# Performance work log

Hardware: AMD Instinct MI355X
Metric: run time of the kernel (lower is better)

## Reference

```python
import jax, jax.numpy as jnp
import numpy as np

DEPTH, HEADS, K, EPS = 4, 8, 3, 1e-5
DIM, CIN, COUT = 128, 64, 64


def conv1x1(x, w, b=None):
    y = jnp.einsum('oi,bihw->bohw', w, x)
    return y if b is None else y + b[None, :, None, None]


def dilated_conv3x3(x, w, b, d):
    y = jax.lax.conv_general_dilated(
        x, w, window_strides=(1, 1), padding=[(d, d), (d, d)],
        rhs_dilation=(d, d), dimension_numbers=('NCHW', 'OIHW', 'NCHW'))
    return y + b[None, :, None, None]


def batchnorm_train(x, g, b):
    # BatchNorm2d in training mode: biased batch stats over (B,H,W)
    mu = jnp.mean(x, axis=(0, 2, 3), keepdims=True)
    var = jnp.var(x, axis=(0, 2, 3), keepdims=True)
    return (x - mu) * jax.lax.rsqrt(var + EPS) * g[None, :, None, None] + b[None, :, None, None]


def unfold3(x):
    # nn.Unfold(k=3, pad=1): (B,C,H,W) -> (B,C,k*k,H,W), patch index row-major (dy,dx)
    B, C, H, W = x.shape
    p = K // 2
    xp = jnp.pad(x, ((0, 0), (0, 0), (p, p), (p, p)))
    return jnp.stack([xp[:, :, dy:dy + H, dx:dx + W]
                      for dy in range(K) for dx in range(K)], axis=2)


def local_self_attention(x, qkv_w, fc_w, fc_b):
    B, C, H, W = x.shape
    c = C // HEADS
    scale = c ** -0.5
    qkv = conv1x1(x, qkv_w)                      # (B,3C,H,W)
    q, k, v = jnp.split(qkv, 3, axis=1)
    shape6 = lambda t: unfold3(t).reshape(B, HEADS, c, K * K, H, W)
    q, k, v = shape6(q) * scale, shape6(k), shape6(v)
    # NOTE: original einsum labels dim2 (channels/head) as n/m and dim3 (k^2) as the
    # contracted axis, i.e. channel-attention contracted over the 9 patch positions.
    dots = jnp.einsum('bhnkij,bhmkij->bhnmij', q, k)   # (B,h,c,c,H,W)
    attn = jax.nn.softmax(dots, axis=3)
    out = jnp.einsum('bhnmij,bhmkij->bhnkij', attn, v)  # (B,h,c,k^2,H,W)
    out = out.reshape(B, C, K * K, H, W).sum(axis=2)
    return conv1x1(out, fc_w, fc_b) + x


def setup_inputs() -> dict:
    key = jax.random.key(0)
    ks = jax.random.split(key, 12)
    s = 0.05
    return {
        'x': jax.random.normal(ks[0], (2, CIN, 96, 96), jnp.float32),
        'w_in': jax.random.normal(ks[1], (DIM, CIN), jnp.float32) * s,
        'b_in': jnp.zeros((DIM,), jnp.float32),
        'conv_w': jax.random.normal(ks[2], (DEPTH, DIM, DIM, 3, 3), jnp.float32) * s,
        'conv_b': jnp.zeros((DEPTH, DIM), jnp.float32),
        'bn_g': jnp.ones((DEPTH, DIM), jnp.float32),
        'bn_b': jnp.zeros((DEPTH, DIM), jnp.float32),
        'qkv_w': jax.random.normal(ks[3], (DEPTH, 3 * DIM, DIM), jnp.float32) * s,
        'fc_w': jax.random.normal(ks[4], (DEPTH, DIM, DIM), jnp.float32) * s,
        'fc_b': jnp.zeros((DEPTH, DIM), jnp.float32),
        'w_out': jax.random.normal(ks[5], (COUT, DIM), jnp.float32) * s,
        'b_out': jnp.zeros((COUT,), jnp.float32),
    }


def reference(x, w_in, b_in, conv_w, conv_b, bn_g, bn_b, qkv_w, fc_w, fc_b, w_out, b_out):
    h = conv1x1(x, w_in, b_in)
    for i in range(DEPTH):
        d = 2 ** i
        h = jax.nn.relu(batchnorm_train(dilated_conv3x3(h, conv_w[i], conv_b[i], d), bn_g[i], bn_b[i]))
        h = local_self_attention(h, qkv_w[i], fc_w[i], fc_b[i])
    return conv1x1(h, w_out, b_out)
```

## Files before the change

### kernel.cpp

```cpp
#include <hip/hip_runtime.h>
#include <math.h>

typedef __attribute__((ext_vector_type(8))) short bf16x8;
typedef __attribute__((ext_vector_type(4))) float f32x4;
typedef __attribute__((ext_vector_type(4))) unsigned short us4;
typedef __attribute__((ext_vector_type(8))) unsigned short us8;

constexpr int BB = 2;
constexpr int CC = 128;
constexpr int HH = 96, WW = 96;
constexpr int PP = HH * WW;
constexpr int NN = BB * PP;
constexpr int CONV_BLKS = NN / 48;

__device__ __forceinline__ float bf2f(unsigned short u) {
    return __uint_as_float(((unsigned)u) << 16);
}
__device__ __forceinline__ unsigned short f2bf(float f) {
    unsigned u = __float_as_uint(f);
    unsigned r = u + 0x7fff + ((u >> 16) & 1);
    return (unsigned short)(r >> 16);
}

__global__ __launch_bounds__(256)
void k_wconv(const float* __restrict__ conv_w, const float* __restrict__ qkv_w,
             const float* __restrict__ fc_w, const float* __restrict__ w_in,
             const float* __restrict__ w_out,
             unsigned short* __restrict__ wcv, unsigned short* __restrict__ wqkv,
             unsigned short* __restrict__ wfc, unsigned short* __restrict__ wi,
             unsigned short* __restrict__ wo)
{
    int gid = blockIdx.x * 256 + threadIdx.x;
    if (gid < 589824) {
        int L = gid / 147456, r = gid % 147456;
        int o = r / 1152, k = r % 1152;
        int t = k / 128, c = k % 128;
        float v = conv_w[(((size_t)(L * 128 + o) * 128 + c) * 9) + t];
        wcv[gid] = f2bf(v);
    } else if (gid < 786432) {
        int g = gid - 589824;
        int o = (g % 49152) / 128;
        float v = qkv_w[g] * (o < 128 ? 0.25f : 1.0f);
        wqkv[g] = f2bf(v);
    } else if (gid < 851968) {
        int g = gid - 786432;
        wfc[g] = f2bf(fc_w[g]);
    } else if (gid < 860160) {
        int g = gid - 851968;
        wi[g] = f2bf(w_in[g]);
    } else if (gid < 868352) {
        int g = gid - 860160;
        wo[g] = f2bf(w_out[g]);
    }
}

__global__ __launch_bounds__(256)
void k_xconv(const float* __restrict__ x, unsigned short* __restrict__ xT)
{
    int n = blockIdx.x * 256 + threadIdx.x;
    int b = n / PP, p = n - b * PP;
    unsigned short* dst = xT + (size_t)n * 64;
    #pragma unroll
    for (int cg = 0; cg < 16; ++cg) {
        us4 st;
        #pragma unroll
        for (int r = 0; r < 4; ++r)
            st[r] = f2bf(x[((size_t)(b * 64 + cg * 4 + r)) * PP + p]);
        *reinterpret_cast<us4*>(dst + cg * 4) = st;
    }
}

template<int DIL>
__global__ __launch_bounds__(192)
void k_conv(const unsigned short* __restrict__ W,
            const unsigned short* __restrict__ act,
            float* __restrict__ y,
            float* __restrict__ parts,
            const unsigned short* __restrict__ zp)
{
    int tid = threadIdx.x;
    int lane = tid & 63, wz = tid >> 6;
    int l15 = lane & 15, kg = lane >> 4;

    int n_base = blockIdx.x * 48;
    int o_base = blockIdx.y * 64;

    const unsigned short* wbase[4];
    #pragma unroll
    for (int fm = 0; fm < 4; ++fm)
        wbase[fm] = W + (size_t)(o_base + fm * 16 + l15) * 1152 + kg * 8;

    const unsigned short* bbase[3];
    int iF[3], jF[3];
    #pragma unroll
    for (int fn = 0; fn < 3; ++fn) {
        int n = n_base + fn * 16 + l15;
        bbase[fn] = act + (size_t)n * 128 + kg * 8;
        int pix = n % PP;
        iF[fn] = pix / WW;
        jF[fn] = pix % WW;
    }

    f32x4 acc[4][3];
    #pragma unroll
    for (int fm = 0; fm < 4; ++fm)
        #pragma unroll
        for (int fn = 0; fn < 3; ++fn)
            acc[fm][fn] = (f32x4){0.f, 0.f, 0.f, 0.f};

    const unsigned short* zpk = zp + kg * 8;
    int t0 = wz * 3;
    #pragma unroll
    for (int tt = 0; tt < 3; ++tt) {
        int t = t0 + tt;
        int oy = (t / 3 - 1) * DIL, ox = (t % 3 - 1) * DIL;
        int disp = (oy * WW + ox) * 128;
        const unsigned short* baddr[3];
        #pragma unroll
        for (int fn = 0; fn < 3; ++fn) {
            bool v = ((unsigned)(iF[fn] + oy) < (unsigned)HH) &&
                     ((unsigned)(jF[fn] + ox) < (unsigned)WW);
            baddr[fn] = v ? (bbase[fn] + disp) : zpk;
        }
        #pragma unroll
        for (int c0 = 0; c0 < 128; c0 += 32) {
            bf16x8 a[4], b[3];
            #pragma unroll
            for (int fm = 0; fm < 4; ++fm)
                a[fm] = *reinterpret_cast<const bf16x8*>(wbase[fm] + t * 128 + c0);
            #pragma unroll
            for (int fn = 0; fn < 3; ++fn)
                b[fn] = *reinterpret_cast<const bf16x8*>(baddr[fn] + c0);
            #pragma unroll
            for (int fm = 0; fm < 4; ++fm)
                #pragma unroll
                for (int fn = 0; fn < 3; ++fn)
                    acc[fm][fn] = __builtin_amdgcn_mfma_f32_16x16x32_bf16(
                        a[fm], b[fn], acc[fm][fn], 0, 0, 0);
        }
    }

    __shared__ float red[2][48][64];
    if (wz) {
        #pragma unroll
        for (int fm = 0; fm < 4; ++fm)
            #pragma unroll
            for (int fn = 0; fn < 3; ++fn)
                #pragma unroll
                for (int r = 0; r < 4; ++r)
                    red[wz - 1][fm * 12 + fn * 4 + r][lane] = acc[fm][fn][r];
    }
    __syncthreads();
    if (wz == 0) {
        #pragma unroll
        for (int fm = 0; fm < 4; ++fm)
            #pragma unroll
            for (int fn = 0; fn < 3; ++fn)
                #pragma unroll
                for (int r = 0; r < 4; ++r)
                    acc[fm][fn][r] += red[0][fm * 12 + fn * 4 + r][lane] +
                                      red[1][fm * 12 + fn * 4 + r][lane];

        #pragma unroll
        for (int fm = 0; fm < 4; ++fm) {
            int o0 = o_base + fm * 16 + kg * 4;
            #pragma unroll
            for (int fn = 0; fn < 3; ++fn) {
                int n = n_base + fn * 16 + l15;
                *reinterpret_cast<f32x4*>(y + (size_t)n * 128 + o0) = acc[fm][fn];
            }
        }

        #pragma unroll
        for (int fm = 0; fm < 4; ++fm) {
            #pragma unroll
            for (int r = 0; r < 4; ++r) {
                float s = 0.f, s2 = 0.f;
                #pragma unroll
                for (int fn = 0; fn < 3; ++fn) {
                    float v = acc[fm][fn][r];
                    s += v; s2 += v * v;
                }
                #pragma unroll
                for (int m = 1; m <= 8; m <<= 1) {
                    s  += __shfl_xor(s,  m, 64);
                    s2 += __shfl_xor(s2, m, 64);
                }
                if (l15 == 0) {
                    int c = o_base + fm * 16 + kg * 4 + r;
                    parts[(size_t)blockIdx.x * 256 + c]       = s;
                    parts[(size_t)blockIdx.x * 256 + 128 + c] = s2;
                }
            }
        }
    }
}

template<int WM, int WN, int F, int MODE>
__global__ __launch_bounds__(WM * WN * 64)
void k_gemm(const unsigned short* __restrict__ W,
            const unsigned short* __restrict__ act,
            const float* __restrict__ bias,
            const unsigned short* __restrict__ resid,
            void* __restrict__ outp,
            int Kw, int Cin, int Cout)
{
    int tid = threadIdx.x;
    int lane = tid & 63, wv = tid >> 6;
    int wm = wv % WM, wn = wv / WM;
    int l15 = lane & 15, kg = lane >> 4;

    int n_base = blockIdx.x * (WN * 16 * F) + wn * 16 * F;
    int o_base = blockIdx.y * (WM * 64) + wm * 64;

    const unsigned short* wbase[4];
    #pragma unroll
    for (int fm = 0; fm < 4; ++fm) {
        int o = o_base + fm * 16 + l15;
        wbase[fm] = W + (size_t)o * Kw + kg * 8;
    }

    const unsigned short* bbase[F];
    #pragma unroll
    for (int fn = 0; fn < F; ++fn) {
        int n = n_base + fn * 16 + l15;
        bbase[fn] = act + (size_t)n * Cin + kg * 8;
    }

    f32x4 acc[4][F];
    #pragma unroll
    for (int fm = 0; fm < 4; ++fm)
        #pragma unroll
        for (int fn = 0; fn < F; ++fn)
            acc[fm][fn] = (f32x4){0.f, 0.f, 0.f, 0.f};

    #pragma unroll
    for (int k0 = 0; k0 < 128; k0 += 32) {
        if (k0 >= Cin) break;
        bf16x8 a[4], b[F];
        #pragma unroll
        for (int fm = 0; fm < 4; ++fm)
            a[fm] = *reinterpret_cast<const bf16x8*>(wbase[fm] + k0);
        #pragma unroll
        for (int fn = 0; fn < F; ++fn)
            b[fn] = *reinterpret_cast<const bf16x8*>(bbase[fn] + k0);
        #pragma unroll
        for (int fm = 0; fm < 4; ++fm)
            #pragma unroll
            for (int fn = 0; fn < F; ++fn)
                acc[fm][fn] = __builtin_amdgcn_mfma_f32_16x16x32_bf16(
                    a[fm], b[fn], acc[fm][fn], 0, 0, 0);
    }

    #pragma unroll
    for (int fm = 0; fm < 4; ++fm) {
        #pragma unroll
        for (int fn = 0; fn < F; ++fn) {
            f32x4 v = acc[fm][fn];
            int n = n_base + fn * 16 + l15;
            int o0 = o_base + fm * 16 + kg * 4;
            if constexpr (MODE == 0 || MODE == 2) {
                if (bias) {
                    #pragma unroll
                    for (int r = 0; r < 4; ++r) v[r] += bias[o0 + r];
                }
                if constexpr (MODE == 2) {
                    us4 rv = *reinterpret_cast<const us4*>(resid + (size_t)n * Cout + o0);
                    #pragma unroll
                    for (int r = 0; r < 4; ++r) v[r] += bf2f(rv[r]);
                }
                us4 st;
                #pragma unroll
                for (int r = 0; r < 4; ++r) st[r] = f2bf(v[r]);
                *reinterpret_cast<us4*>((unsigned short*)outp + (size_t)n * Cout + o0) = st;
            } else {
                int b_ = n / PP, p = n - b_ * PP;
                float* op = (float*)outp;
                #pragma unroll
                for (int r = 0; r < 4; ++r)
                    op[((size_t)(b_ * Cout + o0 + r)) * PP + p] = v[r] + bias[o0 + r];
            }
        }
    }
}

__global__ __launch_bounds__(384)
void k_bnfin(const float* __restrict__ partials, const float* __restrict__ g,
             const float* __restrict__ b, float* __restrict__ scsh)
{
    int c = blockIdx.x;
    int t = threadIdx.x;
    float s  = partials[(size_t)t * 256 + c];
    float s2 = partials[(size_t)t * 256 + 128 + c];
    #pragma unroll
    for (int m = 32; m > 0; m >>= 1) {
        s  += __shfl_down(s,  m, 64);
        s2 += __shfl_down(s2, m, 64);
    }
    __shared__ float ls[6], ls2[6];
    int wid = t >> 6;
    if ((t & 63) == 0) { ls[wid] = s; ls2[wid] = s2; }
    __syncthreads();
    if (t == 0) {
        float S = 0.f, S2 = 0.f;
        #pragma unroll
        for (int w = 0; w < 6; ++w) { S += ls[w]; S2 += ls2[w]; }
        const float inv = 1.f / (float)NN;
        float mu = S * inv;
        float var = S2 * inv - mu * mu;
        float sc = g[c] * rsqrtf(var + 1e-5f);
        scsh[c] = sc;
        scsh[128 + c] = b[c] - mu * sc;
    }
}

__global__ __launch_bounds__(256)
void k_bnrelu(const float* __restrict__ y, const float* __restrict__ scsh,
              unsigned short* __restrict__ h)
{
    int gid = blockIdx.x * 256 + threadIdx.x;
    int c0 = (gid * 4) & 127;
    size_t idx = (size_t)gid * 4;
    f32x4 v = *reinterpret_cast<const f32x4*>(y + idx);
    us4 st;
    #pragma unroll
    for (int r = 0; r < 4; ++r) {
        float f = fmaxf(fmaf(v[r], scsh[c0 + r], scsh[128 + c0 + r]), 0.f);
        st[r] = f2bf(f);
    }
    *reinterpret_cast<us4*>(h + idx) = st;
}

__global__ __launch_bounds__(256)
void k_attn2(const unsigned short* __restrict__ qkv, unsigned short* __restrict__ att)
{
    __shared__ unsigned short tile[288 * 104];
    int tid = threadIdx.x;
    int br = blockIdx.x;
    int hp = blockIdx.y;
    int b = br / HH, i = br - (br / HH) * HH;

    #pragma unroll 1
    for (int it = 0; it < 14; ++it) {
        int idx = it * 256 + tid;
        if (idx < 3456) {
            int pp = idx / 12;
            int rem = idx - pp * 12;
            int s = rem >> 2, u8 = rem & 3;
            int rr = pp / 96, col = pp - rr * 96;
            int ai = i + rr - 1;
            us8 val = {0, 0, 0, 0, 0, 0, 0, 0};
            if ((unsigned)ai < (unsigned)HH) {
                int n = b * PP + ai * WW + col;
                val = *reinterpret_cast<const us8*>(
                    qkv + (size_t)n * 384 + s * 128 + hp * 32 + u8 * 8);
            }
            *reinterpret_cast<us8*>(tile + pp * 104 + s * 32 + u8 * 8) = val;
        }
    }
    __syncthreads();

    #pragma unroll 1
    for (int u = 0; u < 3; ++u) {
        int unit = u * 256 + tid;
        int j  = unit >> 3;
        int h  = (unit >> 2) & 1;
        int ng = unit & 3;

        float dots[4][16];
        float vs[16];
        #pragma unroll
        for (int m = 0; m < 16; ++m) vs[m] = 0.f;
        #pragma unroll
        for (int nn = 0; nn < 4; ++nn)
            #pragma unroll
            for (int m = 0; m < 16; ++m) dots[nn][m] = 0.f;

        #pragma unroll 1
        for (int rr = 0; rr < 3; ++rr) {
            #pragma unroll
            for (int dj = -1; dj <= 1; ++dj) {
                int jj = j + dj;
                if ((unsigned)jj >= (unsigned)WW) continue;
                const unsigned short* pb = tile + (rr * 96 + jj) * 104 + h * 16;
                us4 q4 = *reinterpret_cast<const us4*>(pb + ng * 4);
                us8 k0 = *reinterpret_cast<const us8*>(pb + 32);
                us8 k1 = *reinterpret_cast<const us8*>(pb + 40);
                us8 v0 = *reinterpret_cast<const us8*>(pb + 64);
                us8 v1 = *reinterpret_cast<const us8*>(pb + 72);
                float kf[16];
                #pragma unroll
                for (int e = 0; e < 8; ++e) {
                    kf[e] = bf2f(k0[e]);
                    kf[8 + e] = bf2f(k1[e]);
                    vs[e] += bf2f(v0[e]);
                    vs[8 + e] += bf2f(v1[e]);
                }
                #pragma unroll
                for (int nn = 0; nn < 4; ++nn) {
                    float qf = bf2f(q4[nn]);
                    #pragma unroll
                    for (int m = 0; m < 16; ++m)
                        dots[nn][m] = fmaf(qf, kf[m], dots[nn][m]);
                }
            }
        }

        us4 st;
        #pragma unroll
        for (int nn = 0; nn < 4; ++nn) {
            float mx = dots[nn][0];
            #pragma unroll
            for (int m = 1; m < 16; ++m) mx = fmaxf(mx, dots[nn][m]);
            float den = 0.f, o = 0.f;
            #pragma unroll
            for (int m = 0; m < 16; ++m) {
                float e = __expf(dots[nn][m] - mx);
                den += e;
                o = fmaf(e, vs[m], o);
            }
            st[nn] = f2bf(o / den);
        }
        int n = b * PP + i * WW + j;
        *reinterpret_cast<us4*>(att + (size_t)n * CC + hp * 32 + h * 16 + ng * 4) = st;
    }
}

extern "C" void kernel_launch(void* const* d_in, const int* in_sizes, int n_in,
                              void* d_out, int out_size, void* d_ws, size_t ws_size,
                              hipStream_t stream)
{
    const float* x      = (const float*)d_in[0];
    const float* w_in   = (const float*)d_in[1];
    const float* b_in   = (const float*)d_in[2];
    const float* conv_w = (const float*)d_in[3];
    const float* bn_g   = (const float*)d_in[5];
    const float* bn_b   = (const float*)d_in[6];
    const float* qkv_w  = (const float*)d_in[7];
    const float* fc_w   = (const float*)d_in[8];
    const float* fc_b   = (const float*)d_in[9];
    const float* w_out  = (const float*)d_in[10];
    const float* b_out  = (const float*)d_in[11];

    char* ws = (char*)d_ws;
    unsigned short* zp    = (unsigned short*)(ws);
    unsigned short* wcv   = (unsigned short*)(ws + 4096);
    unsigned short* wqkv  = (unsigned short*)(ws + 1183744);
    unsigned short* wfc   = (unsigned short*)(ws + 1576960);
    unsigned short* wi    = (unsigned short*)(ws + 1708032);
    unsigned short* wo    = (unsigned short*)(ws + 1724416);
    unsigned short* xT    = (unsigned short*)(ws + 1740800);
    unsigned short* bufA  = (unsigned short*)(ws + 4100096);
    float*          ybuf  = (float*)        (ws + 8818688);
    unsigned short* hbuf  = (unsigned short*)(ws + 18255872);
    unsigned short* qkvb  = (unsigned short*)(ws + 22974464);
    unsigned short* attb  = (unsigned short*)(ws + 37130240);
    float*          parts = (float*)        (ws + 41848832);
    float*          scsh  = (float*)        (ws + 42242048);

    hipMemsetAsync(zp, 0, 4096, stream);

    k_wconv<<<3392, 256, 0, stream>>>(conv_w, qkv_w, fc_w, w_in, w_out,
                                      wcv, wqkv, wfc, wi, wo);
    k_xconv<<<NN / 256, 256, 0, stream>>>(x, xT);

    k_gemm<1, 2, 3, 0><<<dim3(192, 2), 128, 0, stream>>>(
        wi, xT, b_in, nullptr, bufA, 64, 64, 128);

    for (int L = 0; L < 4; ++L) {
        const unsigned short* wc = wcv + (size_t)L * 147456;
        switch (L) {
            case 0: k_conv<1><<<dim3(CONV_BLKS, 2), 192, 0, stream>>>(wc, bufA, ybuf, parts, zp); break;
            case 1: k_conv<2><<<dim3(CONV_BLKS, 2), 192, 0, stream>>>(wc, bufA, ybuf, parts, zp); break;
            case 2: k_conv<4><<<dim3(CONV_BLKS, 2), 192, 0, stream>>>(wc, bufA, ybuf, parts, zp); break;
            case 3: k_conv<8><<<dim3(CONV_BLKS, 2), 192, 0, stream>>>(wc, bufA, ybuf, parts, zp); break;
        }
        k_bnfin<<<128, 384, 0, stream>>>(parts, bn_g + L * 128, bn_b + L * 128, scsh);
        k_bnrelu<<<2304, 256, 0, stream>>>(ybuf, scsh, hbuf);

        k_gemm<1, 2, 3, 0><<<dim3(192, 6), 128, 0, stream>>>(
            wqkv + (size_t)L * 49152, hbuf, nullptr, nullptr, qkvb, 128, 128, 384);

        k_attn2<<<dim3(BB * HH, 4), 256, 0, stream>>>(qkvb, attb);

        k_gemm<1, 2, 3, 2><<<dim3(192, 2), 128, 0, stream>>>(
            wfc + (size_t)L * 16384, attb, fc_b + L * 128, hbuf, bufA, 128, 128, 128);
    }

    k_gemm<1, 2, 3, 3><<<dim3(192, 1), 128, 0, stream>>>(
        wo, bufA, b_out, nullptr, (float*)d_out, 128, 128, 64);
}
```

Before: 462.2 us.

## Split conv output channels and attention heads across more blocks, add halo padding

The dilated conv kernel now computes 32 output channels per block instead of 64, doubling the grid in the channel dimension to raise occupancy and parallelism, at the cost of reloading the activation tiles twice as often. The attention kernel now handles one head per block with 192 threads and a tile padded to 98 columns, so the column-boundary branch disappears. It also fully unrolls its loops and accumulates the value sums in a separate pass. This reduces per-block shared memory and divergence but raises block count and may increase register pressure from the unrolling.

```diff
diff --git a/kernel.cpp b/kernel.cpp
--- a/kernel.cpp
+++ b/kernel.cpp
@@ -83,11 +83,11 @@
     int l15 = lane & 15, kg = lane >> 4;
 
     int n_base = blockIdx.x * 48;
-    int o_base = blockIdx.y * 64;
-
-    const unsigned short* wbase[4];
-    #pragma unroll
-    for (int fm = 0; fm < 4; ++fm)
+    int o_base = blockIdx.y * 32;
+
+    const unsigned short* wbase[2];
+    #pragma unroll
+    for (int fm = 0; fm < 2; ++fm)
         wbase[fm] = W + (size_t)(o_base + fm * 16 + l15) * 1152 + kg * 8;
 
     const unsigned short* bbase[3];
@@ -101,9 +101,9 @@
         jF[fn] = pix % WW;
     }
 
-    f32x4 acc[4][3];
-    #pragma unroll
-    for (int fm = 0; fm < 4; ++fm)
+    f32x4 acc[2][3];
+    #pragma unroll
+    for (int fm = 0; fm < 2; ++fm)
         #pragma unroll
         for (int fn = 0; fn < 3; ++fn)
             acc[fm][fn] = (f32x4){0.f, 0.f, 0.f, 0.f};
@@ -124,15 +124,15 @@
         }
         #pragma unroll
         for (int c0 = 0; c0 < 128; c0 += 32) {
-            bf16x8 a[4], b[3];
-            #pragma unroll
-            for (int fm = 0; fm < 4; ++fm)
+            bf16x8 a[2], b[3];
+            #pragma unroll
+            for (int fm = 0; fm < 2; ++fm)
                 a[fm] = *reinterpret_cast<const bf16x8*>(wbase[fm] + t * 128 + c0);
             #pragma unroll
             for (int fn = 0; fn < 3; ++fn)
                 b[fn] = *reinterpret_cast<const bf16x8*>(baddr[fn] + c0);
             #pragma unroll
-            for (int fm = 0; fm < 4; ++fm)
+            for (int fm = 0; fm < 2; ++fm)
                 #pragma unroll
                 for (int fn = 0; fn < 3; ++fn)
                     acc[fm][fn] = __builtin_amdgcn_mfma_f32_16x16x32_bf16(
@@ -140,10 +140,10 @@
         }
     }
 
-    __shared__ float red[2][48][64];
+    __shared__ float red[2][24][64];
     if (wz) {
         #pragma unroll
-        for (int fm = 0; fm < 4; ++fm)
+        for (int fm = 0; fm < 2; ++fm)
             #pragma unroll
             for (int fn = 0; fn < 3; ++fn)
                 #pragma unroll
@@ -153,7 +153,7 @@
     __syncthreads();
     if (wz == 0) {
         #pragma unroll
-        for (int fm = 0; fm < 4; ++fm)
+        for (int fm = 0; fm < 2; ++fm)
             #pragma unroll
             for (int fn = 0; fn < 3; ++fn)
                 #pragma unroll
@@ -162,7 +162,7 @@
                                       red[1][fm * 12 + fn * 4 + r][lane];
 
         #pragma unroll
-        for (int fm = 0; fm < 4; ++fm) {
+        for (int fm = 0; fm < 2; ++fm) {
             int o0 = o_base + fm * 16 + kg * 4;
             #pragma unroll
             for (int fn = 0; fn < 3; ++fn) {
@@ -172,7 +172,7 @@
         }
 
         #pragma unroll
-        for (int fm = 0; fm < 4; ++fm) {
+        for (int fm = 0; fm < 2; ++fm) {
             #pragma unroll
             for (int r = 0; r < 4; ++r) {
                 float s = 0.f, s2 = 0.f;
@@ -331,70 +331,60 @@
     *reinterpret_cast<us4*>(h + idx) = st;
 }
 
-__global__ __launch_bounds__(256)
+__global__ __launch_bounds__(192)
 void k_attn2(const unsigned short* __restrict__ qkv, unsigned short* __restrict__ att)
 {
-    __shared__ unsigned short tile[288 * 104];
+    __shared__ unsigned short tile[294 * 56];
     int tid = threadIdx.x;
     int br = blockIdx.x;
-    int hp = blockIdx.y;
-    int b = br / HH, i = br - (br / HH) * HH;
-
-    #pragma unroll 1
-    for (int it = 0; it < 14; ++it) {
-        int idx = it * 256 + tid;
-        if (idx < 3456) {
-            int pp = idx / 12;
-            int rem = idx - pp * 12;
-            int s = rem >> 2, u8 = rem & 3;
-            int rr = pp / 96, col = pp - rr * 96;
-            int ai = i + rr - 1;
+    int head = blockIdx.y;
+    int b = br / HH, i = br - b * HH;
+
+    #pragma unroll
+    for (int it = 0; it < 10; ++it) {
+        int idx = it * 192 + tid;
+        if (idx < 1764) {
+            int pp = idx / 6;
+            int rem = idx - pp * 6;
+            int s = rem >> 1, u8 = rem & 1;
+            int rr = pp / 98, cc = pp - rr * 98;
+            int ai = i + rr - 1, aj = cc - 1;
             us8 val = {0, 0, 0, 0, 0, 0, 0, 0};
-            if ((unsigned)ai < (unsigned)HH) {
-                int n = b * PP + ai * WW + col;
+            if (((unsigned)ai < (unsigned)HH) && ((unsigned)aj < (unsigned)WW)) {
+                int n = b * PP + ai * WW + aj;
                 val = *reinterpret_cast<const us8*>(
-                    qkv + (size_t)n * 384 + s * 128 + hp * 32 + u8 * 8);
-            }
-            *reinterpret_cast<us8*>(tile + pp * 104 + s * 32 + u8 * 8) = val;
+                    qkv + (size_t)n * 384 + s * 128 + head * 16 + u8 * 8);
+            }
+            *reinterpret_cast<us8*>(tile + pp * 56 + s * 16 + u8 * 8) = val;
         }
     }
     __syncthreads();
 
-    #pragma unroll 1
-    for (int u = 0; u < 3; ++u) {
-        int unit = u * 256 + tid;
-        int j  = unit >> 3;
-        int h  = (unit >> 2) & 1;
+    #pragma unroll
+    for (int u = 0; u < 2; ++u) {
+        int unit = u * 192 + tid;
+        int j  = unit >> 2;
         int ng = unit & 3;
 
         float dots[4][16];
-        float vs[16];
-        #pragma unroll
-        for (int m = 0; m < 16; ++m) vs[m] = 0.f;
         #pragma unroll
         for (int nn = 0; nn < 4; ++nn)
             #pragma unroll
             for (int m = 0; m < 16; ++m) dots[nn][m] = 0.f;
 
-        #pragma unroll 1
+        #pragma unroll
         for (int rr = 0; rr < 3; ++rr) {
             #pragma unroll
-            for (int dj = -1; dj <= 1; ++dj) {
-                int jj = j + dj;
-                if ((unsigned)jj >= (unsigned)WW) continue;
-                const unsigned short* pb = tile + (rr * 96 + jj) * 104 + h * 16;
+            for (int dj = 0; dj < 3; ++dj) {
+                const unsigned short* pb = tile + (rr * 98 + j + dj) * 56;
                 us4 q4 = *reinterpret_cast<const us4*>(pb + ng * 4);
-                us8 k0 = *reinterpret_cast<const us8*>(pb + 32);
-                us8 k1 = *reinterpret_cast<const us8*>(pb + 40);
-                us8 v0 = *reinterpret_cast<const us8*>(pb + 64);
-                us8 v1 = *reinterpret_cast<const us8*>(pb + 72);
+                us8 k0 = *reinterpret_cast<const us8*>(pb + 16);
+                us8 k1 = *reinterpret_cast<const us8*>(pb + 24);
                 float kf[16];
                 #pragma unroll
                 for (int e = 0; e < 8; ++e) {
                     kf[e] = bf2f(k0[e]);
                     kf[8 + e] = bf2f(k1[e]);
-                    vs[e] += bf2f(v0[e]);
-                    vs[8 + e] += bf2f(v1[e]);
                 }
                 #pragma unroll
                 for (int nn = 0; nn < 4; ++nn) {
@@ -406,6 +396,24 @@
             }
         }
 
+        float vs[16];
+        #pragma unroll
+        for (int m = 0; m < 16; ++m) vs[m] = 0.f;
+        #pragma unroll
+        for (int rr = 0; rr < 3; ++rr) {
+            #pragma unroll
+            for (int dj = 0; dj < 3; ++dj) {
+                const unsigned short* pb = tile + (rr * 98 + j + dj) * 56;
+                us8 v0 = *reinterpret_cast<const us8*>(pb + 32);
+                us8 v1 = *reinterpret_cast<const us8*>(pb + 40);
+                #pragma unroll
+                for (int e = 0; e < 8; ++e) {
+                    vs[e] += bf2f(v0[e]);
+                    vs[8 + e] += bf2f(v1[e]);
+                }
+            }
+        }
+
         us4 st;
         #pragma unroll
         for (int nn = 0; nn < 4; ++nn) {
@@ -422,7 +430,7 @@
             st[nn] = f2bf(o / den);
         }
         int n = b * PP + i * WW + j;
-        *reinterpret_cast<us4*>(att + (size_t)n * CC + hp * 32 + h * 16 + ng * 4) = st;
+        *reinterpret_cast<us4*>(att + (size_t)n * CC + head * 16 + ng * 4) = st;
     }
 }
 
@@ -470,10 +478,10 @@
     for (int L = 0; L < 4; ++L) {
         const unsigned short* wc = wcv + (size_t)L * 147456;
         switch (L) {
-            case 0: k_conv<1><<<dim3(CONV_BLKS, 2), 192, 0, stream>>>(wc, bufA, ybuf, parts, zp); break;
-            case 1: k_conv<2><<<dim3(CONV_BLKS, 2), 192, 0, stream>>>(wc, bufA, ybuf, parts, zp); break;
-            case 2: k_conv<4><<<dim3(CONV_BLKS, 2), 192, 0, stream>>>(wc, bufA, ybuf, parts, zp); break;
-            case 3: k_conv<8><<<dim3(CONV_BLKS, 2), 192, 0, stream>>>(wc, bufA, ybuf, parts, zp); break;
+            case 0: k_conv<1><<<dim3(CONV_BLKS, 4), 192, 0, stream>>>(wc, bufA, ybuf, parts, zp); break;
+            case 1: k_conv<2><<<dim3(CONV_BLKS, 4), 192, 0, stream>>>(wc, bufA, ybuf, parts, zp); break;
+            case 2: k_conv<4><<<dim3(CONV_BLKS, 4), 192, 0, stream>>>(wc, bufA, ybuf, parts, zp); break;
+            case 3: k_conv<8><<<dim3(CONV_BLKS, 4), 192, 0, stream>>>(wc, bufA, ybuf, parts, zp); break;
         }
         k_bnfin<<<128, 384, 0, stream>>>(parts, bn_g + L * 128, bn_b + L * 128, scsh);
         k_bnrelu<<<2304, 256, 0, stream>>>(ybuf, scsh, hbuf);
@@ -481,7 +489,7 @@
         k_gemm<1, 2, 3, 0><<<dim3(192, 6), 128, 0, stream>>>(
             wqkv + (size_t)L * 49152, hbuf, nullptr, nullptr, qkvb, 128, 128, 384);
 
-        k_attn2<<<dim3(BB * HH, 4), 256, 0, stream>>>(qkvb, attb);
+        k_attn2<<<dim3(BB * HH, 8), 192, 0, stream>>>(qkvb, attb);
 
         k_gemm<1, 2, 3, 2><<<dim3(192, 2), 128, 0, stream>>>(
             wfc + (size_t)L * 16384, attb, fc_b + L * 128, hbuf, bufA, 128, 128, 128);
```

Result: slower. 481.8 us (+4.2%).
